# Optimization experiments

Hardware: AMD Instinct MI355X
Metric: run time of the kernel (lower is better)

The kernel has to match this reference:

```python
import jax, jax.numpy as jnp
import numpy as np

HID = 512
NB = 20
N = 65536
EPS = 1e-5


def layer_norm(x, g, b):
    m = jnp.mean(x, axis=-1, keepdims=True)
    v = jnp.mean(jnp.square(x - m), axis=-1, keepdims=True)
    return (x - m) * jax.lax.rsqrt(v + EPS) * g + b


def setup_inputs() -> dict:
    key = jax.random.key(0)
    ks = jax.random.split(key, 8)
    s = 0.02
    return {
        "x": jax.random.normal(ks[0], (N, 2), dtype=jnp.float32),
        "in_w": jax.random.normal(ks[1], (2, HID), dtype=jnp.float32) * s,
        "in_b": jnp.zeros((HID,), jnp.float32),
        "ln1_g": jnp.ones((NB, HID), jnp.float32),
        "ln1_b": jnp.zeros((NB, HID), jnp.float32),
        "fc1_w": jax.random.normal(ks[2], (NB, HID, HID), dtype=jnp.float32) * s,
        "fc1_b": jnp.zeros((NB, HID), jnp.float32),
        "ln2_g": jnp.ones((NB, HID), jnp.float32),
        "ln2_b": jnp.zeros((NB, HID), jnp.float32),
        "fc2_w": jax.random.normal(ks[3], (NB, HID, HID), dtype=jnp.float32) * s,
        "fc2_b": jnp.zeros((NB, HID), jnp.float32),
        "out_ln_g": jnp.ones((HID,), jnp.float32),
        "out_ln_b": jnp.zeros((HID,), jnp.float32),
        "out_w": jax.random.normal(ks[4], (HID, 1), dtype=jnp.float32) * s,
        "out_b": jnp.zeros((1,), jnp.float32),
    }


def reference(x, in_w, in_b, ln1_g, ln1_b, fc1_w, fc1_b, ln2_g, ln2_b,
              fc2_w, fc2_b, out_ln_g, out_ln_b, out_w, out_b):
    # in_proj + SiLU: [N,2] @ [2,HID]
    h = jax.nn.silu(x @ in_w + in_b)

    def block(h, p):
        g1, b1, w1, c1, g2, b2, w2, c2 = p
        t = jax.nn.silu(layer_norm(h, g1, b1) @ w1 + c1)
        t = layer_norm(t, g2, b2) @ w2 + c2
        return h + t, None

    h, _ = jax.lax.scan(block, h, (ln1_g, ln1_b, fc1_w, fc1_b,
                                   ln2_g, ln2_b, fc2_w, fc2_b))
    h = jax.nn.silu(layer_norm(h, out_ln_g, out_ln_b))
    return h @ out_w + out_b  # [N, 1]
```

## Files before the change

### kernel.cpp

```cpp
#include <hip/hip_runtime.h>


typedef float  fvec4 __attribute__((ext_vector_type(4)));
typedef __bf16 bvec8 __attribute__((ext_vector_type(8)));

#define HN_STRIDE 520
#define PL_STRIDE 67
#define N_PCOL    256
#define WCHUNK    16384
#define SMEM_BYTES (64*HN_STRIDE*2 + N_PCOL*PL_STRIDE*4 + 64*8)
#define WPK_USHORTS ((size_t)20*2*16*WCHUNK)

__device__ __forceinline__ unsigned int f2bf(float v) {
    unsigned int u = __float_as_uint(v);
    return (u + 0x7fffu + ((u >> 16) & 1u)) >> 16;
}
__device__ __forceinline__ float silu_f(float v) {
    return v * (1.0f / (1.0f + __expf(-v)));
}

__global__ __launch_bounds__(256) void pack_weights(
        const float* __restrict__ w1, const float* __restrict__ w2,
        const float* __restrict__ g1, const float* __restrict__ g2,
        unsigned short* __restrict__ pk) {
    int tid = blockIdx.x * 256 + threadIdx.x;
    int l  = tid & 63;
    int f  = tid >> 6;
    int t  = f & 1;
    int kc = (f >> 1) & 15;
    int w  = (f >> 5) & 15;
    int g  = (f >> 9) & 1;
    int b  = f >> 10;
    const float* src = g ? w2 : w1;
    const float* gs  = (g ? g2 : g1) + b * 512;
    int k0 = kc * 32 + (l >> 4) * 8;
    int n  = w * 32 + (l & 15) * 2 + t;
    const float* s = src + ((size_t)b * 512 + k0) * 512 + n;
    unsigned int r[4];
#pragma unroll
    for (int j = 0; j < 4; ++j) {
        float ga = gs[k0 + 2 * j];
        float gb = gs[k0 + 2 * j + 1];
        unsigned int lo = f2bf(ga * s[(size_t)(2*j) * 512]);
        unsigned int hi = f2bf(gb * s[(size_t)(2*j + 1) * 512]);
        r[j] = lo | (hi << 16);
    }
    *(uint4*)(pk + (size_t)tid * 8) = make_uint4(r[0], r[1], r[2], r[3]);
}

__global__ __launch_bounds__(512) void make_uv(
        const float* __restrict__ w1, const float* __restrict__ w2,
        const float* __restrict__ g1, const float* __restrict__ bl1,
        const float* __restrict__ cb1,
        const float* __restrict__ g2, const float* __restrict__ bl2,
        const float* __restrict__ cb2,
        float* __restrict__ uv) {
    int b = blockIdx.x >> 1, slot = blockIdx.x & 1, n = threadIdx.x;
    const float* W  = (slot ? w2 : w1) + (size_t)b * 512 * 512;
    const float* g  = (slot ? g2 : g1) + b * 512;
    const float* bl = (slot ? bl2 : bl1) + b * 512;
    const float* cb = (slot ? cb2 : cb1) + b * 512;
    float u = 0.f, v = 0.f;
    for (int j = 0; j < 512; ++j) {
        float wv = W[(size_t)j * 512 + n];
        u = fmaf(g[j], wv, u);
        v = fmaf(bl[j], wv, v);
    }
    uv[((b * 2 + slot) * 2 + 0) * 512 + n] = u;
    uv[((b * 2 + slot) * 2 + 1) * 512 + n] = v + cb[n];
}

__device__ __forceinline__ void reduce_mv(const unsigned int* plane,
                                          float2* mv, int tid) {
    int r = tid >> 4, j = tid & 15;
    float s = 0.f, ss = 0.f;
#pragma unroll
    for (int u = 0; u < 16; ++u) {
        unsigned int pv = plane[(j + 16 * u) * PL_STRIDE + r];
        s  += __uint_as_float(pv << 16);
        ss += __uint_as_float(pv & 0xFFFF0000u);
    }
    s += __shfl_xor(s, 1); ss += __shfl_xor(ss, 1);
    s += __shfl_xor(s, 2); ss += __shfl_xor(ss, 2);
    s += __shfl_xor(s, 4); ss += __shfl_xor(ss, 4);
    s += __shfl_xor(s, 8); ss += __shfl_xor(ss, 8);
    if (j == 0) {
        float mean = s * (1.f / 512.f);
        float var  = ss * (1.f / 512.f) - mean * mean;
        mv[r] = make_float2(mean, rsqrtf(var + 1e-5f));
    }
}

__device__ __forceinline__ void do_gemm(fvec4 acc[4][2],
                                        const unsigned short* hn,
                                        const unsigned short* __restrict__ wp,
                                        int l, int c, int q) {
#pragma unroll 2
    for (int kc = 0; kc < 16; ++kc) {
        bvec8 a[4], bb[2];
#pragma unroll
        for (int rb = 0; rb < 4; ++rb)
            a[rb] = *(const bvec8*)(hn + (rb * 16 + c) * HN_STRIDE + kc * 32 + q * 8);
#pragma unroll
        for (int t = 0; t < 2; ++t)
            bb[t] = *(const bvec8*)(wp + (kc * 2 + t) * 512 + l * 8);
#pragma unroll
        for (int rb = 0; rb < 4; ++rb)
#pragma unroll
            for (int t = 0; t < 2; ++t)
                acc[rb][t] = __builtin_amdgcn_mfma_f32_16x16x32_bf16(
                    a[rb], bb[t], acc[rb][t], 0, 0, 0);
    }
}

__global__ __launch_bounds__(1024, 4) void mlp_fused(
        const float* __restrict__ x,
        const float* __restrict__ in_w,  const float* __restrict__ in_b,
        const float* __restrict__ out_ln_g, const float* __restrict__ out_ln_b,
        const float* __restrict__ out_w, const float* __restrict__ out_b,
        const unsigned short* __restrict__ wpk,
        const float* __restrict__ uv,
        float* __restrict__ out) {
    extern __shared__ char smem[];
    unsigned short* hn = (unsigned short*)smem;
    unsigned int* plane = (unsigned int*)(smem + 64 * HN_STRIDE * 2);
    float* planef = (float*)plane;
    float2* mv = (float2*)(smem + 64 * HN_STRIDE * 2 + N_PCOL * PL_STRIDE * 4);

    const int tid = threadIdx.x;
    const int w = tid >> 6;
    const int l = tid & 63, c = l & 15, q = l >> 4;
    const int colbase = w * 32 + c * 2;
    const int pcol = w * 16 + c;
    const int row0 = blockIdx.x * 64;

    float h[4][4][2];

    {
        float2 iw0 = *(const float2*)(in_w + colbase);
        float2 iw1 = *(const float2*)(in_w + 512 + colbase);
        float2 ib  = *(const float2*)(in_b + colbase);
#pragma unroll
        for (int rb = 0; rb < 4; ++rb)
#pragma unroll
            for (int i = 0; i < 4; ++i) {
                int row = rb * 16 + q * 4 + i;
                float2 xv = *(const float2*)(x + (size_t)(row0 + row) * 2);
                h[rb][i][0] = silu_f(xv.x * iw0.x + xv.y * iw1.x + ib.x);
                h[rb][i][1] = silu_f(xv.x * iw0.y + xv.y * iw1.y + ib.y);
            }
    }

    for (int b = 0; b < 20; ++b) {
        float2 u1  = *(const float2*)(uv + ((b * 2 + 0) * 2 + 0) * 512 + colbase);
        float2 vc1 = *(const float2*)(uv + ((b * 2 + 0) * 2 + 1) * 512 + colbase);
        float2 u2  = *(const float2*)(uv + ((b * 2 + 1) * 2 + 0) * 512 + colbase);
        float2 vc2 = *(const float2*)(uv + ((b * 2 + 1) * 2 + 1) * 512 + colbase);

#pragma unroll
        for (int rb = 0; rb < 4; ++rb)
#pragma unroll
            for (int i = 0; i < 4; ++i) {
                int row = rb * 16 + q * 4 + i;
                float v0 = h[rb][i][0], v1 = h[rb][i][1];
                plane[pcol * PL_STRIDE + row] =
                    f2bf(v0 + v1) | (f2bf(__builtin_fmaf(v0, v0, v1 * v1)) << 16);
                *(unsigned int*)(hn + row * HN_STRIDE + colbase) =
                    f2bf(v0) | (f2bf(v1) << 16);
            }
        __syncthreads();
        reduce_mv(plane, mv, tid);

        fvec4 acc[4][2];
#pragma unroll
        for (int rb = 0; rb < 4; ++rb)
#pragma unroll
            for (int t = 0; t < 2; ++t) acc[rb][t] = (fvec4){0.f, 0.f, 0.f, 0.f};
        do_gemm(acc, hn, wpk + ((size_t)(b * 2 + 0) * 16 + w) * WCHUNK, l, c, q);
        __syncthreads();

#pragma unroll
        for (int rb = 0; rb < 4; ++rb)
#pragma unroll
            for (int i = 0; i < 4; ++i) {
                int row = rb * 16 + q * 4 + i;
                float2 m = mv[row];
                float minv = -m.x * m.y;
                float t0 = silu_f(__builtin_fmaf(acc[rb][0][i], m.y,
                                  __builtin_fmaf(minv, u1.x, vc1.x)));
                float t1 = silu_f(__builtin_fmaf(acc[rb][1][i], m.y,
                                  __builtin_fmaf(minv, u1.y, vc1.y)));
                plane[pcol * PL_STRIDE + row] =
                    f2bf(t0 + t1) | (f2bf(__builtin_fmaf(t0, t0, t1 * t1)) << 16);
                *(unsigned int*)(hn + row * HN_STRIDE + colbase) =
                    f2bf(t0) | (f2bf(t1) << 16);
            }
        __syncthreads();
        reduce_mv(plane, mv, tid);

#pragma unroll
        for (int rb = 0; rb < 4; ++rb)
#pragma unroll
            for (int t = 0; t < 2; ++t) acc[rb][t] = (fvec4){0.f, 0.f, 0.f, 0.f};
        do_gemm(acc, hn, wpk + ((size_t)(b * 2 + 1) * 16 + w) * WCHUNK, l, c, q);
        __syncthreads();

#pragma unroll
        for (int rb = 0; rb < 4; ++rb)
#pragma unroll
            for (int i = 0; i < 4; ++i) {
                int row = rb * 16 + q * 4 + i;
                float2 m = mv[row];
                float minv = -m.x * m.y;
                h[rb][i][0] = __builtin_fmaf(acc[rb][0][i], m.y,
                    h[rb][i][0] + __builtin_fmaf(minv, u2.x, vc2.x));
                h[rb][i][1] = __builtin_fmaf(acc[rb][1][i], m.y,
                    h[rb][i][1] + __builtin_fmaf(minv, u2.y, vc2.y));
            }
    }

#pragma unroll
    for (int rb = 0; rb < 4; ++rb)
#pragma unroll
        for (int i = 0; i < 4; ++i) {
            int row = rb * 16 + q * 4 + i;
            float v0 = h[rb][i][0], v1 = h[rb][i][1];
            plane[pcol * PL_STRIDE + row] =
                f2bf(v0 + v1) | (f2bf(__builtin_fmaf(v0, v0, v1 * v1)) << 16);
        }
    __syncthreads();
    reduce_mv(plane, mv, tid);
    __syncthreads();
    {
        float2 og = *(const float2*)(out_ln_g + colbase);
        float2 ob = *(const float2*)(out_ln_b + colbase);
        float2 ow = *(const float2*)(out_w + colbase);
#pragma unroll
        for (int rb = 0; rb < 4; ++rb)
#pragma unroll
            for (int i = 0; i < 4; ++i) {
                int row = rb * 16 + q * 4 + i;
                float2 m = mv[row];
                float v0 = (h[rb][i][0] - m.x) * m.y * og.x + ob.x;
                float v1 = (h[rb][i][1] - m.x) * m.y * og.y + ob.y;
                planef[pcol * PL_STRIDE + row] = silu_f(v0) * ow.x + silu_f(v1) * ow.y;
            }
    }
    __syncthreads();
    {
        int r = tid >> 4, j = tid & 15;
        float s = 0.f;
#pragma unroll
        for (int u = 0; u < 16; ++u)
            s += planef[(j + 16 * u) * PL_STRIDE + r];
        s += __shfl_xor(s, 1);
        s += __shfl_xor(s, 2);
        s += __shfl_xor(s, 4);
        s += __shfl_xor(s, 8);
        if (j == 0) out[row0 + r] = s + out_b[0];
    }
}

extern "C" void kernel_launch(void* const* d_in, const int* in_sizes, int n_in,
                              void* d_out, int out_size, void* d_ws, size_t ws_size,
                              hipStream_t stream) {
    const float* x        = (const float*)d_in[0];
    const float* in_w     = (const float*)d_in[1];
    const float* in_b     = (const float*)d_in[2];
    const float* ln1_g    = (const float*)d_in[3];
    const float* ln1_b    = (const float*)d_in[4];
    const float* fc1_w    = (const float*)d_in[5];
    const float* fc1_b    = (const float*)d_in[6];
    const float* ln2_g    = (const float*)d_in[7];
    const float* ln2_b    = (const float*)d_in[8];
    const float* fc2_w    = (const float*)d_in[9];
    const float* fc2_b    = (const float*)d_in[10];
    const float* out_ln_g = (const float*)d_in[11];
    const float* out_ln_b = (const float*)d_in[12];
    const float* out_w    = (const float*)d_in[13];
    const float* out_b    = (const float*)d_in[14];
    float* out = (float*)d_out;
    unsigned short* wpk = (unsigned short*)d_ws;
    float* uv = (float*)((char*)d_ws + WPK_USHORTS * 2);

    (void)hipFuncSetAttribute((const void*)mlp_fused,
                              hipFuncAttributeMaxDynamicSharedMemorySize, SMEM_BYTES);

    pack_weights<<<5120, 256, 0, stream>>>(fc1_w, fc2_w, ln1_g, ln2_g, wpk);
    make_uv<<<40, 512, 0, stream>>>(fc1_w, fc2_w, ln1_g, ln1_b, fc1_b,
                                    ln2_g, ln2_b, fc2_b, uv);
    mlp_fused<<<1024, 1024, SMEM_BYTES, stream>>>(
        x, in_w, in_b, out_ln_g, out_ln_b, out_w, out_b, wpk, uv, out);
}
```

Before: 1.990 ms.

## Fuse LayerNorm stats reduction into GEMM loop reading bf16 activations from hn

Removes the separate partial-sum plane in shared memory. Row mean and variance are now computed directly from the bf16 activation tile, interleaved into kc iterations 4-7 of the fully unrolled MFMA loop, so the stats work overlaps the matrix math and one block-wide reduce phase goes away. It also prefetches the first weight fragments before the barrier and uses a packed bf16 conversion intrinsic. This shrinks LDS use, which may allow more blocks per CU, but the full unroll adds register pressure. Computing the stats from rounded bf16 values changes numerics slightly.

```diff
diff --git a/kernel.cpp b/kernel.cpp
--- a/kernel.cpp
+++ b/kernel.cpp
@@ -1,19 +1,24 @@
 #include <hip/hip_runtime.h>
+#include <hip/hip_bf16.h>
 
 
 typedef float  fvec4 __attribute__((ext_vector_type(4)));
 typedef __bf16 bvec8 __attribute__((ext_vector_type(8)));
 
 #define HN_STRIDE 520
-#define PL_STRIDE 67
-#define N_PCOL    256
 #define WCHUNK    16384
-#define SMEM_BYTES (64*HN_STRIDE*2 + N_PCOL*PL_STRIDE*4 + 64*8)
+#define SMEM_BYTES (64*HN_STRIDE*2 + 64*8)
 #define WPK_USHORTS ((size_t)20*2*16*WCHUNK)
 
 __device__ __forceinline__ unsigned int f2bf(float v) {
     unsigned int u = __float_as_uint(v);
     return (u + 0x7fffu + ((u >> 16) & 1u)) >> 16;
+}
+__device__ __forceinline__ unsigned int pkbf(float a, float b) {
+    __hip_bfloat162 t = __float22bfloat162_rn(make_float2(a, b));
+    unsigned int r;
+    __builtin_memcpy(&r, &t, 4);
+    return r;
 }
 __device__ __forceinline__ float silu_f(float v) {
     return v * (1.0f / (1.0f + __expf(-v)));
@@ -70,15 +75,46 @@
     uv[((b * 2 + slot) * 2 + 1) * 512 + n] = v + cb[n];
 }
 
-__device__ __forceinline__ void reduce_mv(const unsigned int* plane,
-                                          float2* mv, int tid) {
-    int r = tid >> 4, j = tid & 15;
+__device__ __forceinline__ void acc_u32(unsigned int u, float& s, float& ss) {
+    float lo = __uint_as_float(u << 16);
+    float hi = __uint_as_float(u & 0xFFFF0000u);
+    s += lo + hi;
+    ss = __builtin_fmaf(lo, lo, ss);
+    ss = __builtin_fmaf(hi, hi, ss);
+}
+
+__device__ __forceinline__ void gemm_red(
+        fvec4 acc[4][2], const unsigned short* hn,
+        const unsigned short* __restrict__ wp, uint4 pre0, uint4 pre1,
+        float2* mv, int l, int c, int q, int tid) {
+    const uint4* wp4 = (const uint4*)wp;
+    const int r = tid >> 4, j = tid & 15;
     float s = 0.f, ss = 0.f;
 #pragma unroll
-    for (int u = 0; u < 16; ++u) {
-        unsigned int pv = plane[(j + 16 * u) * PL_STRIDE + r];
-        s  += __uint_as_float(pv << 16);
-        ss += __uint_as_float(pv & 0xFFFF0000u);
+    for (int kc = 0; kc < 16; ++kc) {
+        bvec8 a[4], b0, b1;
+#pragma unroll
+        for (int rb = 0; rb < 4; ++rb)
+            a[rb] = *(const bvec8*)(hn + (rb * 16 + c) * HN_STRIDE + kc * 32 + q * 8);
+        if (kc == 0) {
+            __builtin_memcpy(&b0, &pre0, 16);
+            __builtin_memcpy(&b1, &pre1, 16);
+        } else {
+            uint4 r0 = wp4[(kc * 2 + 0) * 64 + l];
+            uint4 r1 = wp4[(kc * 2 + 1) * 64 + l];
+            __builtin_memcpy(&b0, &r0, 16);
+            __builtin_memcpy(&b1, &r1, 16);
+        }
+        if (kc >= 4 && kc < 8) {
+            uint4 pv = *(const uint4*)(hn + r * HN_STRIDE + (j + 16 * (kc - 4)) * 8);
+            acc_u32(pv.x, s, ss); acc_u32(pv.y, s, ss);
+            acc_u32(pv.z, s, ss); acc_u32(pv.w, s, ss);
+        }
+#pragma unroll
+        for (int rb = 0; rb < 4; ++rb) {
+            acc[rb][0] = __builtin_amdgcn_mfma_f32_16x16x32_bf16(a[rb], b0, acc[rb][0], 0, 0, 0);
+            acc[rb][1] = __builtin_amdgcn_mfma_f32_16x16x32_bf16(a[rb], b1, acc[rb][1], 0, 0, 0);
+        }
     }
     s += __shfl_xor(s, 1); ss += __shfl_xor(ss, 1);
     s += __shfl_xor(s, 2); ss += __shfl_xor(ss, 2);
@@ -91,25 +127,24 @@
     }
 }
 
-__device__ __forceinline__ void do_gemm(fvec4 acc[4][2],
-                                        const unsigned short* hn,
-                                        const unsigned short* __restrict__ wp,
-                                        int l, int c, int q) {
-#pragma unroll 2
-    for (int kc = 0; kc < 16; ++kc) {
-        bvec8 a[4], bb[2];
-#pragma unroll
-        for (int rb = 0; rb < 4; ++rb)
-            a[rb] = *(const bvec8*)(hn + (rb * 16 + c) * HN_STRIDE + kc * 32 + q * 8);
-#pragma unroll
-        for (int t = 0; t < 2; ++t)
-            bb[t] = *(const bvec8*)(wp + (kc * 2 + t) * 512 + l * 8);
-#pragma unroll
-        for (int rb = 0; rb < 4; ++rb)
-#pragma unroll
-            for (int t = 0; t < 2; ++t)
-                acc[rb][t] = __builtin_amdgcn_mfma_f32_16x16x32_bf16(
-                    a[rb], bb[t], acc[rb][t], 0, 0, 0);
+__device__ __forceinline__ void reduce_mv_hn(const unsigned short* hn,
+                                             float2* mv, int tid) {
+    int r = tid >> 4, j = tid & 15;
+    float s = 0.f, ss = 0.f;
+#pragma unroll
+    for (int u = 0; u < 4; ++u) {
+        uint4 pv = *(const uint4*)(hn + r * HN_STRIDE + (j + 16 * u) * 8);
+        acc_u32(pv.x, s, ss); acc_u32(pv.y, s, ss);
+        acc_u32(pv.z, s, ss); acc_u32(pv.w, s, ss);
+    }
+    s += __shfl_xor(s, 1); ss += __shfl_xor(ss, 1);
+    s += __shfl_xor(s, 2); ss += __shfl_xor(ss, 2);
+    s += __shfl_xor(s, 4); ss += __shfl_xor(ss, 4);
+    s += __shfl_xor(s, 8); ss += __shfl_xor(ss, 8);
+    if (j == 0) {
+        float mean = s * (1.f / 512.f);
+        float var  = ss * (1.f / 512.f) - mean * mean;
+        mv[r] = make_float2(mean, rsqrtf(var + 1e-5f));
     }
 }
 
@@ -123,15 +158,13 @@
         float* __restrict__ out) {
     extern __shared__ char smem[];
     unsigned short* hn = (unsigned short*)smem;
-    unsigned int* plane = (unsigned int*)(smem + 64 * HN_STRIDE * 2);
-    float* planef = (float*)plane;
-    float2* mv = (float2*)(smem + 64 * HN_STRIDE * 2 + N_PCOL * PL_STRIDE * 4);
+    float* hnf = (float*)smem;
+    float2* mv = (float2*)(smem + 64 * HN_STRIDE * 2);
 
     const int tid = threadIdx.x;
     const int w = tid >> 6;
     const int l = tid & 63, c = l & 15, q = l >> 4;
     const int colbase = w * 32 + c * 2;
-    const int pcol = w * 16 + c;
     const int row0 = blockIdx.x * 64;
 
     float h[4][4][2];
@@ -152,33 +185,35 @@
     }
 
     for (int b = 0; b < 20; ++b) {
+        const unsigned short* wp1 = wpk + ((size_t)(b * 2 + 0) * 16 + w) * WCHUNK;
+        const unsigned short* wp2 = wpk + ((size_t)(b * 2 + 1) * 16 + w) * WCHUNK;
         float2 u1  = *(const float2*)(uv + ((b * 2 + 0) * 2 + 0) * 512 + colbase);
         float2 vc1 = *(const float2*)(uv + ((b * 2 + 0) * 2 + 1) * 512 + colbase);
         float2 u2  = *(const float2*)(uv + ((b * 2 + 1) * 2 + 0) * 512 + colbase);
         float2 vc2 = *(const float2*)(uv + ((b * 2 + 1) * 2 + 1) * 512 + colbase);
 
-#pragma unroll
-        for (int rb = 0; rb < 4; ++rb)
-#pragma unroll
-            for (int i = 0; i < 4; ++i) {
-                int row = rb * 16 + q * 4 + i;
-                float v0 = h[rb][i][0], v1 = h[rb][i][1];
-                plane[pcol * PL_STRIDE + row] =
-                    f2bf(v0 + v1) | (f2bf(__builtin_fmaf(v0, v0, v1 * v1)) << 16);
+        uint4 pre0 = ((const uint4*)wp1)[l];
+        uint4 pre1 = ((const uint4*)wp1)[64 + l];
+#pragma unroll
+        for (int rb = 0; rb < 4; ++rb)
+#pragma unroll
+            for (int i = 0; i < 4; ++i) {
+                int row = rb * 16 + q * 4 + i;
                 *(unsigned int*)(hn + row * HN_STRIDE + colbase) =
-                    f2bf(v0) | (f2bf(v1) << 16);
+                    pkbf(h[rb][i][0], h[rb][i][1]);
             }
         __syncthreads();
-        reduce_mv(plane, mv, tid);
 
         fvec4 acc[4][2];
 #pragma unroll
         for (int rb = 0; rb < 4; ++rb)
 #pragma unroll
             for (int t = 0; t < 2; ++t) acc[rb][t] = (fvec4){0.f, 0.f, 0.f, 0.f};
-        do_gemm(acc, hn, wpk + ((size_t)(b * 2 + 0) * 16 + w) * WCHUNK, l, c, q);
+        gemm_red(acc, hn, wp1, pre0, pre1, mv, l, c, q, tid);
         __syncthreads();
 
+        pre0 = ((const uint4*)wp2)[l];
+        pre1 = ((const uint4*)wp2)[64 + l];
 #pragma unroll
         for (int rb = 0; rb < 4; ++rb)
 #pragma unroll
@@ -190,19 +225,15 @@
                                   __builtin_fmaf(minv, u1.x, vc1.x)));
                 float t1 = silu_f(__builtin_fmaf(acc[rb][1][i], m.y,
                                   __builtin_fmaf(minv, u1.y, vc1.y)));
-                plane[pcol * PL_STRIDE + row] =
-                    f2bf(t0 + t1) | (f2bf(__builtin_fmaf(t0, t0, t1 * t1)) << 16);
-                *(unsigned int*)(hn + row * HN_STRIDE + colbase) =
-                    f2bf(t0) | (f2bf(t1) << 16);
+                *(unsigned int*)(hn + row * HN_STRIDE + colbase) = pkbf(t0, t1);
             }
         __syncthreads();
-        reduce_mv(plane, mv, tid);
 
 #pragma unroll
         for (int rb = 0; rb < 4; ++rb)
 #pragma unroll
             for (int t = 0; t < 2; ++t) acc[rb][t] = (fvec4){0.f, 0.f, 0.f, 0.f};
-        do_gemm(acc, hn, wpk + ((size_t)(b * 2 + 1) * 16 + w) * WCHUNK, l, c, q);
+        gemm_red(acc, hn, wp2, pre0, pre1, mv, l, c, q, tid);
         __syncthreads();
 
 #pragma unroll
@@ -224,26 +255,26 @@
 #pragma unroll
         for (int i = 0; i < 4; ++i) {
             int row = rb * 16 + q * 4 + i;
-            float v0 = h[rb][i][0], v1 = h[rb][i][1];
-            plane[pcol * PL_STRIDE + row] =
-                f2bf(v0 + v1) | (f2bf(__builtin_fmaf(v0, v0, v1 * v1)) << 16);
+            *(unsigned int*)(hn + row * HN_STRIDE + colbase) =
+                pkbf(h[rb][i][0], h[rb][i][1]);
         }
     __syncthreads();
-    reduce_mv(plane, mv, tid);
+    reduce_mv_hn(hn, mv, tid);
     __syncthreads();
     {
         float2 og = *(const float2*)(out_ln_g + colbase);
         float2 ob = *(const float2*)(out_ln_b + colbase);
         float2 ow = *(const float2*)(out_w + colbase);
-#pragma unroll
-        for (int rb = 0; rb < 4; ++rb)
+        const int pcol = w * 16 + c;
+#pragma unroll
+    for (int rb = 0; rb < 4; ++rb)
 #pragma unroll
             for (int i = 0; i < 4; ++i) {
                 int row = rb * 16 + q * 4 + i;
                 float2 m = mv[row];
                 float v0 = (h[rb][i][0] - m.x) * m.y * og.x + ob.x;
                 float v1 = (h[rb][i][1] - m.x) * m.y * og.y + ob.y;
-                planef[pcol * PL_STRIDE + row] = silu_f(v0) * ow.x + silu_f(v1) * ow.y;
+                hnf[pcol * 65 + row] = silu_f(v0) * ow.x + silu_f(v1) * ow.y;
             }
     }
     __syncthreads();
@@ -252,7 +283,7 @@
         float s = 0.f;
 #pragma unroll
         for (int u = 0; u < 16; ++u)
-            s += planef[(j + 16 * u) * PL_STRIDE + r];
+            s += hnf[(j + 16 * u) * 65 + r];
         s += __shfl_xor(s, 1);
         s += __shfl_xor(s, 2);
         s += __shfl_xor(s, 4);
```

New measurement: 1.776 ms. 10.7% less time.
